# Optimization experiments

Hardware: AMD Instinct MI355X
Metric: run time of the kernel (lower is better)

## Reference

```python
import jax, jax.numpy as jnp
import numpy as np

B, S, V, H = 1, 2048, 1024, 16
D = V // H  # head_size = 64


def setup_inputs() -> dict:
    key = jax.random.key(0)
    ks = jax.random.split(key, 7)
    s = 1.0 / np.sqrt(V)  # keep logits in a sane range
    return {
        "x": jax.random.normal(ks[0], (B, S, V), jnp.float32),
        "W_qkv": (jax.random.normal(ks[1], (3 * V, V), jnp.float32) * s),
        "W_out": (jax.random.normal(ks[2], (V, V), jnp.float32) * s),
        "W_pos": (jax.random.normal(ks[3], (V, V), jnp.float32) * s),
        "u_vec": (jax.random.normal(ks[4], (1, H, 1, D), jnp.float32) * 0.02),
        "v_vec": (jax.random.normal(ks[5], (1, H, 1, D), jnp.float32) * 0.02),
        "rel_embed": jax.random.normal(ks[6], (S, V), jnp.float32),
    }


def reference(x, W_qkv, W_out, W_pos, u_vec, v_vec, rel_embed):
    b, s, _ = x.shape
    # qkv projection (nn.Linear, no bias): x @ W.T, then split into q,k,v
    qkv = x @ W_qkv.T
    q, k, v = jnp.split(qkv, 3, axis=-1)
    to_heads = lambda t: t.reshape(b, s, H, D).transpose(0, 2, 1, 3)  # [B,H,S,D]
    q, k, v = to_heads(q), to_heads(k), to_heads(v)

    # content term: (q + u) @ k^T  -> [B,H,S,S]
    attn_dots = jnp.einsum('bhid,bhjd->bhij', q + u_vec, k)

    # relative-position term: Linear(rel_embed).T viewed as [H, D, S]
    rel = (rel_embed @ W_pos.T).T.reshape(H, D, s)
    query_posn = jnp.einsum('bhid,hdj->bhij', q + v_vec, rel)  # [B,H,S,S]

    # Transformer-XL style shift-gather: out[i, j] = in[i, (j - i - 1) mod S]
    col_idx = ((-jnp.arange(s))[:, None] + jnp.arange(s)[None, :] - 1) % s
    shifted = jnp.take_along_axis(query_posn, col_idx[None, None, :, :], axis=-1)

    causal_mask = jnp.triu(jnp.ones((s, s), dtype=bool), k=1)  # True above diagonal
    dots = jnp.where(causal_mask, -jnp.inf, attn_dots + shifted) / np.sqrt(D)
    scores = jax.nn.softmax(dots, axis=-1)

    attn = jnp.einsum('bhij,bhjd->bhid', scores, v)
    out = attn.transpose(0, 2, 1, 3).reshape(b, s, V) @ W_out.T
    return out
```

## Files before the change

kernel.cpp:

```cpp
#include <hip/hip_runtime.h>
#include <math.h>

#define S 2048
#define H 16
#define D 64
#define V 1024

typedef float f32x4 __attribute__((ext_vector_type(4)));
typedef __bf16 bf16x8 __attribute__((ext_vector_type(8)));
typedef unsigned short u16;

#define GLOBAL_AS __attribute__((address_space(1)))
#define LDS_AS __attribute__((address_space(3)))

__device__ __forceinline__ u16 f2bf(float x) {
    unsigned u = __float_as_uint(x);
    u = u + 0x7FFFu + ((u >> 16) & 1u);
    return (u16)(u >> 16);
}
__device__ __forceinline__ float bf2f(u16 b) {
    return __uint_as_float(((unsigned)b) << 16);
}

#if __has_builtin(__builtin_amdgcn_global_load_lds)
#define HAS_ASYNC 1
#endif

__device__ __forceinline__ void async_ld16(const u16* g, u16* ldsu, int lane) {
#ifdef HAS_ASYNC
    auto gp = reinterpret_cast<GLOBAL_AS void*>(reinterpret_cast<uintptr_t>(g));
    auto lp = reinterpret_cast<LDS_AS void*>(reinterpret_cast<uintptr_t>(ldsu));
    __builtin_amdgcn_global_load_lds(gp, lp, 16, 0, 0);
#else
    *(uint4*)((char*)ldsu + lane * 16) = *(const uint4*)g;
#endif
}

__global__ __launch_bounds__(256) void prep5(
    const float* __restrict__ a0, u16* __restrict__ b0, int n0,
    const float* __restrict__ a1, u16* __restrict__ b1, int n1,
    const float* __restrict__ a2, u16* __restrict__ b2, int n2,
    const float* __restrict__ a3, u16* __restrict__ b3, int n3,
    const float* __restrict__ a4, u16* __restrict__ b4, int n4)
{
    const int tot = n0 + n1 + n2 + n3 + n4;
    for (int i = blockIdx.x * 256 + threadIdx.x; i < tot; i += gridDim.x * 256) {
        const float* s; u16* d; int j = i;
        if (j < n0) { s = a0; d = b0; }
        else if ((j -= n0) < n1) { s = a1; d = b1; }
        else if ((j -= n1) < n2) { s = a2; d = b2; }
        else if ((j -= n2) < n3) { s = a3; d = b3; }
        else { j -= n3; s = a4; d = b4; }
        float4 f = ((const float4*)s)[j];
        ((ushort4*)d)[j] = make_ushort4(f2bf(f.x), f2bf(f.y), f2bf(f.z), f2bf(f.w));
    }
}

__global__ __launch_bounds__(256) void gemm_proj(
    const u16* __restrict__ x_h, const u16* __restrict__ rel_h,
    const u16* __restrict__ Wq_h, const u16* __restrict__ Wpos_h,
    u16* __restrict__ qk_h, u16* __restrict__ Vt_g, u16* __restrict__ P_h)
{
    __shared__ u16 A_s[2][128 * 64];
    __shared__ u16 B_s[2][128 * 64];

    const int bid = (blockIdx.x & 7) * 64 + (blockIdx.x >> 3);
    const bool g1 = bid < 384;
    const int m0 = (g1 ? (bid / 24) : ((bid - 384) / 8)) * 128;
    const int n0 = (g1 ? (bid % 24) : ((bid - 384) % 8)) * 128;
    const u16* Ag = g1 ? x_h : rel_h;
    const u16* Bg = g1 ? Wq_h : Wpos_h;

    const int tid = threadIdx.x;
    const int lane = tid & 63;
    const int w = tid >> 6;
    const int wm = (w & 1) * 64, wn = (w >> 1) * 64;
    const int fr = lane & 15;
    const int fq = lane >> 4;
    const int sr = lane >> 3;
    const int scl = ((lane & 7) ^ sr) * 8;

    auto stage = [&](int k0, int b) {
#pragma unroll
        for (int i = 0; i < 4; ++i) {
            const int r0 = w * 32 + i * 8;
            async_ld16(Ag + (size_t)(m0 + r0 + sr) * 1024 + k0 + scl, A_s[b] + r0 * 64, lane);
            async_ld16(Bg + (size_t)(n0 + r0 + sr) * 1024 + k0 + scl, B_s[b] + r0 * 64, lane);
        }
    };

    f32x4 acc[4][4] = {};

    stage(0, 0);
    for (int kt = 0; kt < 16; ++kt) {
        __syncthreads();
        if (kt + 1 < 16) stage((kt + 1) * 64, (kt + 1) & 1);
        const u16* As = A_s[kt & 1];
        const u16* Bs = B_s[kt & 1];
#pragma unroll
        for (int c = 0; c < 2; ++c) {
            const int ps = ((c * 4 + fq) ^ (fr & 7)) * 8;
            bf16x8 a[4], b[4];
#pragma unroll
            for (int t = 0; t < 4; ++t) {
                a[t] = *(const bf16x8*)&As[(wm + t * 16 + fr) * 64 + ps];
                b[t] = *(const bf16x8*)&Bs[(wn + t * 16 + fr) * 64 + ps];
            }
#pragma unroll
            for (int mi = 0; mi < 4; ++mi)
#pragma unroll
                for (int ni = 0; ni < 4; ++ni)
                    acc[mi][ni] = __builtin_amdgcn_mfma_f32_16x16x32_bf16(
                        a[mi], b[ni], acc[mi][ni], 0, 0, 0);
        }
    }

    const int er = fq * 4;
    if (g1 && n0 >= 2048) {
#pragma unroll
        for (int mi = 0; mi < 4; ++mi)
#pragma unroll
            for (int ni = 0; ni < 4; ++ni) {
                const int col = n0 - 2048 + wn + ni * 16 + fr;
                const int mrow = m0 + wm + mi * 16 + er;
                *(ushort4*)&Vt_g[(size_t)col * 2048 + mrow] = make_ushort4(
                    f2bf(acc[mi][ni][0]), f2bf(acc[mi][ni][1]),
                    f2bf(acc[mi][ni][2]), f2bf(acc[mi][ni][3]));
            }
    } else {
        u16* Cb = g1 ? qk_h : P_h;
        const int ldc = g1 ? 2048 : 1024;
#pragma unroll
        for (int mi = 0; mi < 4; ++mi)
#pragma unroll
            for (int ni = 0; ni < 4; ++ni)
#pragma unroll
                for (int g = 0; g < 4; ++g)
                    Cb[(size_t)(m0 + wm + mi * 16 + er + g) * ldc + n0 + wn + ni * 16 + fr] =
                        f2bf(acc[mi][ni][g]);
    }
}

__global__ __launch_bounds__(256, 2) void attn_mfma(
    const u16* __restrict__ qk_h, const u16* __restrict__ Vt_g,
    const u16* __restrict__ P_h,
    const float* __restrict__ u_vec, const float* __restrict__ v_vec,
    u16* __restrict__ O_h)
{
    const int h = blockIdx.y;
    const int tile = ((blockIdx.y >> 3) & 1) ? blockIdx.x : (gridDim.x - 1 - blockIdx.x);
    const int i0 = tile * 64;
    const int tid = threadIdx.x;
    const int lane = tid & 63;
    const int w = tid >> 6;
    const int fr = lane & 15;
    const int fq = lane >> 4;

    __shared__ u16 K_s[2][64 * 72];
    __shared__ u16 Vt_s[2][64 * 72];
    __shared__ u16 P_s[3][64 * 72];
    __shared__ u16 p_s[64 * 72];

    bf16x8 qu[2], qv[2];
    {
        const int row = i0 + w * 16 + fr;
        const int base = h * 64 + fq * 8;
#pragma unroll
        for (int c = 0; c < 2; ++c) {
            bf16x8 q8 = *(const bf16x8*)(qk_h + (size_t)row * 2048 + base + c * 32);
            float4 u0 = *(const float4*)(u_vec + base + c * 32);
            float4 u1 = *(const float4*)(u_vec + base + c * 32 + 4);
            float4 v0 = *(const float4*)(v_vec + base + c * 32);
            float4 v1 = *(const float4*)(v_vec + base + c * 32 + 4);
            const float uf[8] = {u0.x, u0.y, u0.z, u0.w, u1.x, u1.y, u1.z, u1.w};
            const float vf[8] = {v0.x, v0.y, v0.z, v0.w, v1.x, v1.y, v1.z, v1.w};
#pragma unroll
            for (int j = 0; j < 8; ++j) {
                const float qf = (float)q8[j];
                qu[c][j] = (__bf16)(qf + uf[j]);
                qv[c][j] = (__bf16)(qf + vf[j]);
            }
        }
    }

    const int rKV = tid >> 2;
    const int cKV = (tid & 3) * 16;
    const int rP = tid >> 2;
    const int cP = (tid & 3) * 16;

    uint4 pfK0, pfK1, pfV0, pfV1, pfP0, pfP1;
    auto load_pf = [&](int j0) {
        const u16* kg = qk_h + (size_t)(j0 + rKV) * 2048 + 1024 + h * 64 + cKV;
        pfK0 = *(const uint4*)kg;
        pfK1 = *(const uint4*)(kg + 8);
        const u16* vg = Vt_g + (size_t)(h * 64 + rKV) * 2048 + j0 + cKV;
        pfV0 = *(const uint4*)vg;
        pfV1 = *(const uint4*)(vg + 8);
        int prow = S + j0 - i0 + rP;
        if (prow > S - 1) prow = S - 1;
        const u16* pg = P_h + (size_t)prow * 1024 + h * 64 + cP;
        pfP0 = *(const uint4*)pg;
        pfP1 = *(const uint4*)(pg + 8);
    };

    {
        const int prow = S - i0 - 64 + rP;
        const u16* pg = P_h + (size_t)prow * 1024 + h * 64 + cP;
        *(uint4*)&P_s[0][rP * 72 + cP] = *(const uint4*)pg;
        *(uint4*)&P_s[0][rP * 72 + cP + 8] = *(const uint4*)(pg + 8);
    }
    load_pf(0);
    *(uint4*)&K_s[0][rKV * 72 + cKV] = pfK0;
    *(uint4*)&K_s[0][rKV * 72 + cKV + 8] = pfK1;
    *(uint4*)&Vt_s[0][rKV * 72 + cKV] = pfV0;
    *(uint4*)&Vt_s[0][rKV * 72 + cKV + 8] = pfV1;
    *(uint4*)&P_s[1][rP * 72 + cP] = pfP0;
    *(uint4*)&P_s[1][rP * 72 + cP + 8] = pfP1;
    if (i0 >= 64) load_pf(64);

    u16 *Kcur = K_s[0], *Knxt = K_s[1];
    u16 *Vcur = Vt_s[0], *Vnxt = Vt_s[1];
    u16 *Plo = P_s[0], *Phi = P_s[1], *Pwr = P_s[2];

    f32x4 O[4] = {};
    float l[4] = {};

    const int tbase = 3 - w;
    const int bsh = 15 - fq * 4;

    __syncthreads();

    for (int j0 = 0; j0 <= i0; j0 += 64) {
        if (j0 + 64 <= i0) {
            *(uint4*)&Knxt[rKV * 72 + cKV] = pfK0;
            *(uint4*)&Knxt[rKV * 72 + cKV + 8] = pfK1;
            *(uint4*)&Vnxt[rKV * 72 + cKV] = pfV0;
            *(uint4*)&Vnxt[rKV * 72 + cKV + 8] = pfV1;
            *(uint4*)&Pwr[rP * 72 + cP] = pfP0;
            *(uint4*)&Pwr[rP * 72 + cP + 8] = pfP1;
        }
        if (j0 + 128 <= i0) load_pf(j0 + 128);

        f32x4 accQK[4] = {};
        f32x4 accQP[5] = {};
#pragma unroll
        for (int c = 0; c < 2; ++c) {
            const int kk = c * 32 + fq * 8;
#pragma unroll
            for (int nt = 0; nt < 4; ++nt) {
                bf16x8 b = *(const bf16x8*)&Kcur[(nt * 16 + fr) * 72 + kk];
                accQK[nt] = __builtin_amdgcn_mfma_f32_16x16x32_bf16(qu[c], b, accQK[nt], 0, 0, 0);
            }
#pragma unroll
            for (int t = 0; t < 5; ++t) {
                const int s = tbase + t;
                const u16* Pb = (s < 4) ? Plo : Phi;
                bf16x8 b = *(const bf16x8*)&Pb[((s & 3) * 16 + fr) * 72 + kk];
                accQP[t] = __builtin_amdgcn_mfma_f32_16x16x32_bf16(qv[c], b, accQP[t], 0, 0, 0);
            }
        }

        float p[4][4];
#pragma unroll
        for (int nt = 0; nt < 4; ++nt)
#pragma unroll
            for (int g = 0; g < 4; ++g) {
                const int b = bsh - g;
                const int srcLane = (fq << 4) | ((fr + b) & 15);
                const float sv = (fr >= b) ? accQP[nt][g] : accQP[nt + 1][g];
                const float qp = __shfl(sv, srcLane, 64);
                const int rr = w * 16 + fq * 4 + g;
                const int j = nt * 16 + fr;
                const float s = (accQK[nt][g] + qp) * 0.125f;
                const float e = ((j0 + j) <= (i0 + rr)) ? __expf(s) : 0.f;
                p[nt][g] = e;
                l[g] += e;
            }
#pragma unroll
        for (int nt = 0; nt < 4; ++nt)
#pragma unroll
            for (int g = 0; g < 4; ++g)
                p_s[(w * 16 + fq * 4 + g) * 72 + nt * 16 + fr] = f2bf(p[nt][g]);

#pragma unroll
        for (int c = 0; c < 2; ++c) {
            const int kk = c * 32 + fq * 8;
            bf16x8 a = *(const bf16x8*)&p_s[(w * 16 + fr) * 72 + kk];
#pragma unroll
            for (int nt = 0; nt < 4; ++nt) {
                bf16x8 b = *(const bf16x8*)&Vcur[(nt * 16 + fr) * 72 + kk];
                O[nt] = __builtin_amdgcn_mfma_f32_16x16x32_bf16(a, b, O[nt], 0, 0, 0);
            }
        }

        __syncthreads();
        { u16* t0 = Kcur; Kcur = Knxt; Knxt = t0; }
        { u16* t1 = Vcur; Vcur = Vnxt; Vnxt = t1; }
        { u16* t2 = Plo; Plo = Phi; Phi = Pwr; Pwr = t2; }
    }

#pragma unroll
    for (int g = 0; g < 4; ++g)
#pragma unroll
        for (int off = 1; off < 16; off <<= 1)
            l[g] += __shfl_xor(l[g], off, 64);

#pragma unroll
    for (int nt = 0; nt < 4; ++nt)
#pragma unroll
        for (int g = 0; g < 4; ++g) {
            const int rr = w * 16 + fq * 4 + g;
            O_h[(size_t)(i0 + rr) * 1024 + h * 64 + nt * 16 + fr] = f2bf(O[nt][g] / l[g]);
        }
}

__global__ __launch_bounds__(256) void gemm_out(
    const u16* __restrict__ O_g, const u16* __restrict__ Wout_h,
    float* __restrict__ C)
{
    __shared__ u16 A_s[2][64 * 32];
    __shared__ u16 B_s[2][64 * 32];

    const int lin = (blockIdx.x & 7) * 64 + (blockIdx.x >> 3);
    const int m0 = (lin >> 4) * 64, n0 = (lin & 15) * 64;

    const int tid = threadIdx.x;
    const int lane = tid & 63;
    const int w = tid >> 6;
    const int wm = (w & 1) * 32, wn = (w >> 1) * 32;
    const int fr = lane & 15;
    const int fq = lane >> 4;
    const int lr = lane >> 2, lc = (lane & 3) * 8;

    auto stage = [&](int k0, int bi) {
        async_ld16(O_g + (size_t)(m0 + w * 16 + lr) * 1024 + k0 + lc,
                   A_s[bi] + w * 16 * 32, lane);
        async_ld16(Wout_h + (size_t)(n0 + w * 16 + lr) * 1024 + k0 + lc,
                   B_s[bi] + w * 16 * 32, lane);
    };

    f32x4 acc[2][2] = {};

    stage(0, 0);
    for (int kt = 0; kt < 32; ++kt) {
        __syncthreads();
        if (kt + 1 < 32) stage((kt + 1) * 32, (kt + 1) & 1);
        const u16* As = A_s[kt & 1];
        const u16* Bs = B_s[kt & 1];

        bf16x8 a[2], b[2];
#pragma unroll
        for (int t = 0; t < 2; ++t) {
            a[t] = *(const bf16x8*)&As[(wm + t * 16 + fr) * 32 + fq * 8];
            b[t] = *(const bf16x8*)&Bs[(wn + t * 16 + fr) * 32 + fq * 8];
        }
#pragma unroll
        for (int mi = 0; mi < 2; ++mi)
#pragma unroll
            for (int ni = 0; ni < 2; ++ni)
                acc[mi][ni] = __builtin_amdgcn_mfma_f32_16x16x32_bf16(
                    a[mi], b[ni], acc[mi][ni], 0, 0, 0);
    }

    const int er = fq * 4;
#pragma unroll
    for (int mi = 0; mi < 2; ++mi)
#pragma unroll
        for (int ni = 0; ni < 2; ++ni)
#pragma unroll
            for (int g = 0; g < 4; ++g)
                C[(size_t)(m0 + wm + mi * 16 + er + g) * 1024 + n0 + wn + ni * 16 + fr] =
                    acc[mi][ni][g];
}

extern "C" void kernel_launch(void* const* d_in, const int* in_sizes, int n_in,
                              void* d_out, int out_size, void* d_ws, size_t ws_size,
                              hipStream_t stream) {
    const float* x     = (const float*)d_in[0];
    const float* W_qkv = (const float*)d_in[1];
    const float* W_out = (const float*)d_in[2];
    const float* W_pos = (const float*)d_in[3];
    const float* u_vec = (const float*)d_in[4];
    const float* v_vec = (const float*)d_in[5];
    const float* rel   = (const float*)d_in[6];
    float* out = (float*)d_out;

    char* ws = (char*)d_ws;
    u16* x_h    = (u16*)(ws);
    u16* rel_h  = (u16*)(ws + 4194304);
    u16* Wq_h   = (u16*)(ws + 8388608);
    u16* Wpos_h = (u16*)(ws + 14680064);
    u16* Wout_h = (u16*)(ws + 16777216);
    u16* qk_h   = (u16*)(ws + 18874368);
    u16* Vt_g   = (u16*)(ws + 27262976);
    u16* P_h    = (u16*)(ws + 31457280);
    u16* O_h    = (u16*)(ws + 35651584);

    prep5<<<dim3(2048), dim3(256), 0, stream>>>(
        x, x_h, 2048 * 1024 / 4,
        rel, rel_h, 2048 * 1024 / 4,
        W_qkv, Wq_h, 3072 * 1024 / 4,
        W_pos, Wpos_h, 1024 * 1024 / 4,
        W_out, Wout_h, 1024 * 1024 / 4);

    gemm_proj<<<dim3(512), dim3(256), 0, stream>>>(
        x_h, rel_h, Wq_h, Wpos_h, qk_h, Vt_g, P_h);

    attn_mfma<<<dim3(32, 16), dim3(256), 0, stream>>>(
        qk_h, Vt_g, P_h, u_vec, v_vec, O_h);

    gemm_out<<<dim3(512), dim3(256), 0, stream>>>(O_h, Wout_h, out);
}
```

Before: 177.1 us.

## Load K and positional fragments directly from global into registers, bypassing LDS

```diff
diff --git a/kernel.cpp b/kernel.cpp
--- a/kernel.cpp
+++ b/kernel.cpp
@@ -156,9 +156,7 @@
     const int fr = lane & 15;
     const int fq = lane >> 4;
 
-    __shared__ u16 K_s[2][64 * 72];
     __shared__ u16 Vt_s[2][64 * 72];
-    __shared__ u16 P_s[3][64 * 72];
     __shared__ u16 p_s[64 * 72];
 
     bf16x8 qu[2], qv[2];
@@ -185,80 +183,75 @@
 
     const int rKV = tid >> 2;
     const int cKV = (tid & 3) * 16;
-    const int rP = tid >> 2;
-    const int cP = (tid & 3) * 16;
-
-    uint4 pfK0, pfK1, pfV0, pfV1, pfP0, pfP1;
-    auto load_pf = [&](int j0) {
-        const u16* kg = qk_h + (size_t)(j0 + rKV) * 2048 + 1024 + h * 64 + cKV;
-        pfK0 = *(const uint4*)kg;
-        pfK1 = *(const uint4*)(kg + 8);
+
+    uint4 pfV0, pfV1;
+    auto load_pfV = [&](int j0) {
         const u16* vg = Vt_g + (size_t)(h * 64 + rKV) * 2048 + j0 + cKV;
         pfV0 = *(const uint4*)vg;
         pfV1 = *(const uint4*)(vg + 8);
-        int prow = S + j0 - i0 + rP;
-        if (prow > S - 1) prow = S - 1;
-        const u16* pg = P_h + (size_t)prow * 1024 + h * 64 + cP;
-        pfP0 = *(const uint4*)pg;
-        pfP1 = *(const uint4*)(pg + 8);
     };
 
-    {
-        const int prow = S - i0 - 64 + rP;
-        const u16* pg = P_h + (size_t)prow * 1024 + h * 64 + cP;
-        *(uint4*)&P_s[0][rP * 72 + cP] = *(const uint4*)pg;
-        *(uint4*)&P_s[0][rP * 72 + cP + 8] = *(const uint4*)(pg + 8);
-    }
-    load_pf(0);
-    *(uint4*)&K_s[0][rKV * 72 + cKV] = pfK0;
-    *(uint4*)&K_s[0][rKV * 72 + cKV + 8] = pfK1;
+    const int tbase = 3 - w;
+    const int bsh = 15 - fq * 4;
+
+    bf16x8 kb[4][2];
+    auto load_kb = [&](int j0) {
+#pragma unroll
+        for (int nt = 0; nt < 4; ++nt) {
+            const u16* kg = qk_h + (size_t)(j0 + nt * 16 + fr) * 2048 + 1024 + h * 64 + fq * 8;
+            kb[nt][0] = *(const bf16x8*)kg;
+            kb[nt][1] = *(const bf16x8*)(kg + 32);
+        }
+    };
+
+    bf16x8 pb[5][2];
+    auto load_pb = [&](int j0) {
+        const int wb = S + j0 - i0 - 64;
+#pragma unroll
+        for (int t = 0; t < 5; ++t) {
+            int prow = wb + (tbase + t) * 16 + fr;
+            if (prow > S - 1) prow = S - 1;
+            const u16* pg = P_h + (size_t)prow * 1024 + h * 64 + fq * 8;
+            pb[t][0] = *(const bf16x8*)pg;
+            pb[t][1] = *(const bf16x8*)(pg + 32);
+        }
+    };
+
+    load_kb(0);
+    load_pb(0);
+    load_pfV(0);
     *(uint4*)&Vt_s[0][rKV * 72 + cKV] = pfV0;
     *(uint4*)&Vt_s[0][rKV * 72 + cKV + 8] = pfV1;
-    *(uint4*)&P_s[1][rP * 72 + cP] = pfP0;
-    *(uint4*)&P_s[1][rP * 72 + cP + 8] = pfP1;
-    if (i0 >= 64) load_pf(64);
-
-    u16 *Kcur = K_s[0], *Knxt = K_s[1];
+    if (i0 >= 64) load_pfV(64);
+
     u16 *Vcur = Vt_s[0], *Vnxt = Vt_s[1];
-    u16 *Plo = P_s[0], *Phi = P_s[1], *Pwr = P_s[2];
 
     f32x4 O[4] = {};
     float l[4] = {};
 
-    const int tbase = 3 - w;
-    const int bsh = 15 - fq * 4;
-
     __syncthreads();
 
     for (int j0 = 0; j0 <= i0; j0 += 64) {
         if (j0 + 64 <= i0) {
-            *(uint4*)&Knxt[rKV * 72 + cKV] = pfK0;
-            *(uint4*)&Knxt[rKV * 72 + cKV + 8] = pfK1;
             *(uint4*)&Vnxt[rKV * 72 + cKV] = pfV0;
             *(uint4*)&Vnxt[rKV * 72 + cKV + 8] = pfV1;
-            *(uint4*)&Pwr[rP * 72 + cP] = pfP0;
-            *(uint4*)&Pwr[rP * 72 + cP + 8] = pfP1;
-        }
-        if (j0 + 128 <= i0) load_pf(j0 + 128);
+        }
+        if (j0 + 128 <= i0) load_pfV(j0 + 128);
 
         f32x4 accQK[4] = {};
         f32x4 accQP[5] = {};
 #pragma unroll
         for (int c = 0; c < 2; ++c) {
-            const int kk = c * 32 + fq * 8;
-#pragma unroll
-            for (int nt = 0; nt < 4; ++nt) {
-                bf16x8 b = *(const bf16x8*)&Kcur[(nt * 16 + fr) * 72 + kk];
-                accQK[nt] = __builtin_amdgcn_mfma_f32_16x16x32_bf16(qu[c], b, accQK[nt], 0, 0, 0);
-            }
-#pragma unroll
-            for (int t = 0; t < 5; ++t) {
-                const int s = tbase + t;
-                const u16* Pb = (s < 4) ? Plo : Phi;
-                bf16x8 b = *(const bf16x8*)&Pb[((s & 3) * 16 + fr) * 72 + kk];
-                accQP[t] = __builtin_amdgcn_mfma_f32_16x16x32_bf16(qv[c], b, accQP[t], 0, 0, 0);
-            }
-        }
+#pragma unroll
+            for (int nt = 0; nt < 4; ++nt)
+                accQK[nt] = __builtin_amdgcn_mfma_f32_16x16x32_bf16(
+                    qu[c], kb[nt][c], accQK[nt], 0, 0, 0);
+#pragma unroll
+            for (int t = 0; t < 5; ++t)
+                accQP[t] = __builtin_amdgcn_mfma_f32_16x16x32_bf16(
+                    qv[c], pb[t][c], accQP[t], 0, 0, 0);
+        }
+        if (j0 + 64 <= i0) { load_kb(j0 + 64); load_pb(j0 + 64); }
 
         float p[4][4];
 #pragma unroll
@@ -294,9 +287,7 @@
         }
 
         __syncthreads();
-        { u16* t0 = Kcur; Kcur = Knxt; Knxt = t0; }
         { u16* t1 = Vcur; Vcur = Vnxt; Vnxt = t1; }
-        { u16* t2 = Plo; Plo = Phi; Phi = Pwr; Pwr = t2; }
     }
 
 #pragma unroll
```

New measurement: 212.3 us. +19.9%, slower.
